# Kernel tuning notes

Measured on AMD Instinct MI355X. Metric: run time of the kernel, lower is better.

The kernel has to match this reference:

```python
import jax, jax.numpy as jnp
import numpy as np

D_MODEL = 1024
NUM_HEADS = 16
HEAD_DIM = D_MODEL // NUM_HEADS


def setup_inputs() -> dict:
    key = jax.random.key(0)
    ks = jax.random.split(key, 9)
    s = 1.0 / np.sqrt(D_MODEL)
    x = jax.random.normal(ks[0], (2, 2048, D_MODEL), dtype=jnp.float32)
    Wq = jax.random.uniform(ks[1], (D_MODEL, D_MODEL), jnp.float32, -s, s)
    bq = jax.random.uniform(ks[2], (D_MODEL,), jnp.float32, -s, s)
    Wk = jax.random.uniform(ks[3], (D_MODEL, D_MODEL), jnp.float32, -s, s)
    bk = jax.random.uniform(ks[4], (D_MODEL,), jnp.float32, -s, s)
    Wv = jax.random.uniform(ks[5], (D_MODEL, D_MODEL), jnp.float32, -s, s)
    bv = jax.random.uniform(ks[6], (D_MODEL,), jnp.float32, -s, s)
    Wo = jax.random.uniform(ks[7], (D_MODEL, D_MODEL), jnp.float32, -s, s)
    bo = jax.random.uniform(ks[8], (D_MODEL,), jnp.float32, -s, s)
    return {"x": x, "Wq": Wq, "bq": bq, "Wk": Wk, "bk": bk,
            "Wv": Wv, "bv": bv, "Wo": Wo, "bo": bo}


def reference(x, Wq, bq, Wk, bk, Wv, bv, Wo, bo):
    B, S, D = x.shape
    H, Hd = NUM_HEADS, HEAD_DIM
    # projections (torch Linear: x @ W.T + b; here W stored as [in, out])
    q = (x @ Wq + bq).reshape(B, S, H, Hd).transpose(0, 2, 1, 3)  # [B,H,S,Hd]
    k = (x @ Wk + bk).reshape(B, S, H, Hd).transpose(0, 2, 1, 3)
    v = (x @ Wv + bv).reshape(B, S, H, Hd).transpose(0, 2, 1, 3)
    scale = 1.0 / jnp.sqrt(jnp.asarray(Hd, dtype=x.dtype))
    scores = jnp.einsum('bhqd,bhkd->bhqk', q, k) * scale  # [B,H,S,S]
    attn = jax.nn.softmax(scores, axis=-1)
    out = jnp.einsum('bhqk,bhkd->bhqd', attn, v)  # [B,H,S,Hd]
    out = out.transpose(0, 2, 1, 3).reshape(B, S, D)
    return out @ Wo + bo
```

## Files before the change

kernel.cpp:

```cpp
#include <hip/hip_runtime.h>
#include <hip/hip_bf16.h>
#include <string.h>


#define DM 1024
#define S_LEN 2048
#define NH 16
#define HD 64

using u16 = unsigned short;
using u32 = unsigned int;

typedef short bf16x8 __attribute__((ext_vector_type(8)));
typedef float f32x4  __attribute__((ext_vector_type(4)));

__device__ __forceinline__ u16 f2bf(float f) {
    u32 i = __float_as_uint(f);
    u32 r = i + 0x7fffu + ((i >> 16) & 1u);
    return (u16)(r >> 16);
}
__device__ __forceinline__ u32 pk_bf16(float a, float b) {
    __hip_bfloat162 h = __float22bfloat162_rn(float2{a, b});
    u32 r; memcpy(&r, &h, 4);
    return r;
}

__global__ __launch_bounds__(256) void prep_x(const float* __restrict__ X, u16* __restrict__ out) {
    int i = (blockIdx.x * 256 + threadIdx.x) * 4;
    float4 v = *(const float4*)(X + i);
    *(uint2*)(out + i) = make_uint2(pk_bf16(v.x, v.y), pk_bf16(v.z, v.w));
}

__global__ __launch_bounds__(256) void prep_wt3(
    const float* __restrict__ W0, const float* __restrict__ W1, const float* __restrict__ W2,
    u16* __restrict__ T0, u16* __restrict__ T1, u16* __restrict__ T2)
{
    __shared__ u16 tile[64][72];
    const float* W = (blockIdx.z == 0) ? W0 : (blockIdx.z == 1) ? W1 : W2;
    u16* WT        = (blockIdx.z == 0) ? T0 : (blockIdx.z == 1) ? T1 : T2;
    const int t = threadIdx.x;
    const int n0 = blockIdx.x * 64, k0 = blockIdx.y * 64;
    #pragma unroll
    for (int it = 0; it < 4; it++) {
        int k = it * 16 + (t >> 4);
        int n = (t & 15) * 4;
        float4 v = *(const float4*)(W + (size_t)(k0 + k) * DM + n0 + n);
        tile[n + 0][k] = f2bf(v.x);
        tile[n + 1][k] = f2bf(v.y);
        tile[n + 2][k] = f2bf(v.z);
        tile[n + 3][k] = f2bf(v.w);
    }
    __syncthreads();
    int n = t >> 2, kg = (t & 3) * 16;
    uint4 a = *(const uint4*)&tile[n][kg];
    uint4 b = *(const uint4*)&tile[n][kg + 8];
    *(uint4*)(WT + (size_t)(n0 + n) * DM + k0 + kg)     = a;
    *(uint4*)(WT + (size_t)(n0 + n) * DM + k0 + kg + 8) = b;
}

__global__ __launch_bounds__(256) void prep_wt1(const float* __restrict__ W, u16* __restrict__ WT) {
    __shared__ u16 tile[64][72];
    const int t = threadIdx.x;
    const int n0 = blockIdx.x * 64, k0 = blockIdx.y * 64;
    #pragma unroll
    for (int it = 0; it < 4; it++) {
        int k = it * 16 + (t >> 4);
        int n = (t & 15) * 4;
        float4 v = *(const float4*)(W + (size_t)(k0 + k) * DM + n0 + n);
        tile[n + 0][k] = f2bf(v.x);
        tile[n + 1][k] = f2bf(v.y);
        tile[n + 2][k] = f2bf(v.z);
        tile[n + 3][k] = f2bf(v.w);
    }
    __syncthreads();
    int n = t >> 2, kg = (t & 3) * 16;
    uint4 a = *(const uint4*)&tile[n][kg];
    uint4 b = *(const uint4*)&tile[n][kg + 8];
    *(uint4*)(WT + (size_t)(n0 + n) * DM + k0 + kg)     = a;
    *(uint4*)(WT + (size_t)(n0 + n) * DM + k0 + kg + 8) = b;
}

__global__ __launch_bounds__(256) void gemm_qkv(
    const u16* __restrict__ WQT, const u16* __restrict__ WKT, const u16* __restrict__ WVT,
    const u16* __restrict__ X,
    const float* __restrict__ bq, const float* __restrict__ bk, const float* __restrict__ bv,
    u16* __restrict__ outQ, u16* __restrict__ outK, u16* __restrict__ outVT)
{
    __shared__ u16 Xs[128][72];
    __shared__ u16 Ws[3][64][72];

    const int t = threadIdx.x;
    const int w = t >> 6, lane = t & 63, quad = lane >> 4, l16 = lane & 15;
    const int Mb0 = blockIdx.x * 64;
    const int Nb0 = blockIdx.y * 128;
    const int Mb = Mb0 + (w & 1) * 32;
    const int Nb = Nb0 + (w >> 1) * 64;
    const int mloc = (w & 1) * 32, nloc = (w >> 1) * 64;

    f32x4 acc[3][2][4];
    #pragma unroll
    for (int q = 0; q < 3; q++)
        #pragma unroll
        for (int i = 0; i < 2; i++)
            #pragma unroll
            for (int j = 0; j < 4; j++) acc[q][i][j] = (f32x4){0.f, 0.f, 0.f, 0.f};

    const int sr = t >> 3, sc8 = (t & 7) * 8;

    for (int k0 = 0; k0 < DM; k0 += 64) {
        __syncthreads();
        #pragma unroll
        for (int i = 0; i < 4; i++) {
            int r = i * 32 + sr;
            *(uint4*)&Xs[r][sc8] =
                *(const uint4*)(X + (size_t)(Nb0 + r) * DM + k0 + sc8);
        }
        #pragma unroll
        for (int i = 0; i < 2; i++) {
            int r = i * 32 + sr;
            *(uint4*)&Ws[0][r][sc8] = *(const uint4*)(WQT + (size_t)(Mb0 + r) * DM + k0 + sc8);
            *(uint4*)&Ws[1][r][sc8] = *(const uint4*)(WKT + (size_t)(Mb0 + r) * DM + k0 + sc8);
            *(uint4*)&Ws[2][r][sc8] = *(const uint4*)(WVT + (size_t)(Mb0 + r) * DM + k0 + sc8);
        }
        __syncthreads();

        #pragma unroll
        for (int ks = 0; ks < 2; ks++) {
            const int kk = ks * 32 + quad * 8;
            bf16x8 bf[4];
            #pragma unroll
            for (int nt = 0; nt < 4; nt++)
                bf[nt] = *(const bf16x8*)&Xs[nloc + nt * 16 + l16][kk];
            bf16x8 aq0 = *(const bf16x8*)&Ws[0][mloc + l16][kk];
            bf16x8 aq1 = *(const bf16x8*)&Ws[0][mloc + 16 + l16][kk];
            bf16x8 ak0 = *(const bf16x8*)&Ws[1][mloc + l16][kk];
            bf16x8 ak1 = *(const bf16x8*)&Ws[1][mloc + 16 + l16][kk];
            bf16x8 av0 = *(const bf16x8*)&Ws[2][mloc + l16][kk];
            bf16x8 av1 = *(const bf16x8*)&Ws[2][mloc + 16 + l16][kk];
            #pragma unroll
            for (int nt = 0; nt < 4; nt++) {
                acc[0][0][nt] = __builtin_amdgcn_mfma_f32_16x16x32_bf16(aq0, bf[nt], acc[0][0][nt], 0, 0, 0);
                acc[0][1][nt] = __builtin_amdgcn_mfma_f32_16x16x32_bf16(aq1, bf[nt], acc[0][1][nt], 0, 0, 0);
                acc[1][0][nt] = __builtin_amdgcn_mfma_f32_16x16x32_bf16(ak0, bf[nt], acc[1][0][nt], 0, 0, 0);
                acc[1][1][nt] = __builtin_amdgcn_mfma_f32_16x16x32_bf16(ak1, bf[nt], acc[1][1][nt], 0, 0, 0);
                acc[2][0][nt] = __builtin_amdgcn_mfma_f32_16x16x32_bf16(av0, bf[nt], acc[2][0][nt], 0, 0, 0);
                acc[2][1][nt] = __builtin_amdgcn_mfma_f32_16x16x32_bf16(av1, bf[nt], acc[2][1][nt], 0, 0, 0);
            }
        }
    }

    const float QS = 0.18033688f;
    #pragma unroll
    for (int mt = 0; mt < 2; mt++) {
        int nf0 = Mb + mt * 16 + quad * 4;
        int h = nf0 >> 6, hd = nf0 & 63;
        float4 bvq = *(const float4*)(bq + nf0);
        float4 bvk = *(const float4*)(bk + nf0);
        #pragma unroll
        for (int nt = 0; nt < 4; nt++) {
            int m = Nb + nt * 16 + l16;
            int b = m >> 11, s = m & 2047;
            size_t idx = (size_t)(b * NH + h) * 131072 + (size_t)s * 64 + hd;
            *(uint2*)(outQ + idx) = make_uint2(
                pk_bf16((acc[0][mt][nt][0] + bvq.x) * QS, (acc[0][mt][nt][1] + bvq.y) * QS),
                pk_bf16((acc[0][mt][nt][2] + bvq.z) * QS, (acc[0][mt][nt][3] + bvq.w) * QS));
            *(uint2*)(outK + idx) = make_uint2(
                pk_bf16(acc[1][mt][nt][0] + bvk.x, acc[1][mt][nt][1] + bvk.y),
                pk_bf16(acc[1][mt][nt][2] + bvk.z, acc[1][mt][nt][3] + bvk.w));
        }
    }
    #pragma unroll
    for (int mt = 0; mt < 2; mt++) {
        #pragma unroll
        for (int r = 0; r < 4; r++) {
            int nf = Mb + mt * 16 + quad * 4 + r;
            int h = nf >> 6, hd = nf & 63;
            float bb = bv[nf];
            #pragma unroll
            for (int nt = 0; nt < 4; nt++) {
                int m = Nb + nt * 16 + l16;
                int b = m >> 11, s = m & 2047;
                outVT[(size_t)(b * NH + h) * 131072 + (size_t)hd * S_LEN + s]
                    = f2bf(acc[2][mt][nt][r] + bb);
            }
        }
    }
}

__global__ __launch_bounds__(256) void gemm_out(
    const u16* __restrict__ A, const u16* __restrict__ B,
    const float* __restrict__ bias, float* __restrict__ of32)
{
    __shared__ u16 As[64][72];
    __shared__ u16 Bs[128][72];

    const int t = threadIdx.x;
    const int w = t >> 6, lane = t & 63, quad = lane >> 4, l16 = lane & 15;
    const int Mb0 = blockIdx.x * 64;
    const int Nb0 = blockIdx.y * 128;
    const int Mb = Mb0 + (w & 1) * 32;
    const int Nb = Nb0 + (w >> 1) * 64;
    const int mloc = (w & 1) * 32, nloc = (w >> 1) * 64;

    f32x4 acc[2][4];
    #pragma unroll
    for (int i = 0; i < 2; i++)
        #pragma unroll
        for (int j = 0; j < 4; j++) acc[i][j] = (f32x4){0.f, 0.f, 0.f, 0.f};

    const int sr = t >> 3, sc8 = (t & 7) * 8;

    for (int k0 = 0; k0 < DM; k0 += 64) {
        const int h = k0 >> 6;
        __syncthreads();
        #pragma unroll
        for (int i = 0; i < 2; i++) {
            int r = i * 32 + sr;
            *(uint4*)&As[r][sc8] = *(const uint4*)(A + (size_t)(Mb0 + r) * DM + k0 + sc8);
        }
        #pragma unroll
        for (int i = 0; i < 4; i++) {
            int r = i * 32 + sr;
            int m = Nb0 + r;
            int b = m >> 11, s = m & 2047;
            *(uint4*)&Bs[r][sc8] =
                *(const uint4*)(B + (size_t)(b * NH + h) * 131072 + (size_t)s * 64 + sc8);
        }
        __syncthreads();

        #pragma unroll
        for (int ks = 0; ks < 2; ks++) {
            const int kk = ks * 32 + quad * 8;
            bf16x8 a0 = *(const bf16x8*)&As[mloc + l16][kk];
            bf16x8 a1 = *(const bf16x8*)&As[mloc + 16 + l16][kk];
            #pragma unroll
            for (int nt = 0; nt < 4; nt++) {
                bf16x8 bf = *(const bf16x8*)&Bs[nloc + nt * 16 + l16][kk];
                acc[0][nt] = __builtin_amdgcn_mfma_f32_16x16x32_bf16(a0, bf, acc[0][nt], 0, 0, 0);
                acc[1][nt] = __builtin_amdgcn_mfma_f32_16x16x32_bf16(a1, bf, acc[1][nt], 0, 0, 0);
            }
        }
    }
    #pragma unroll
    for (int mt = 0; mt < 2; mt++) {
        int nf0 = Mb + mt * 16 + quad * 4;
        float4 bvv = *(const float4*)(bias + nf0);
        #pragma unroll
        for (int nt = 0; nt < 4; nt++) {
            int m = Nb + nt * 16 + l16;
            float4 o;
            o.x = acc[mt][nt][0] + bvv.x; o.y = acc[mt][nt][1] + bvv.y;
            o.z = acc[mt][nt][2] + bvv.z; o.w = acc[mt][nt][3] + bvv.w;
            *(float4*)(of32 + (size_t)m * DM + nf0) = o;
        }
    }
}

__global__ __launch_bounds__(512) void attn_mfma(
    const u16* __restrict__ Q, const u16* __restrict__ K, const u16* __restrict__ VT,
    u16* __restrict__ O)
{
    __shared__ u16 Ks[2][64][72];
    __shared__ u16 Vs[2][64][72];
    __shared__ u16 P[128][72];

    const int t = threadIdx.x;
    const int w = t >> 6, lane = t & 63, quad = lane >> 4, l16 = lane & 15;
    const int bh = blockIdx.y;
    const int q0 = blockIdx.x * 128;
    const size_t base = (size_t)bh * 131072;

    bf16x8 qf[2];
    qf[0] = *(const bf16x8*)(Q + base + (size_t)(q0 + w * 16 + l16) * 64 + quad * 8);
    qf[1] = *(const bf16x8*)(Q + base + (size_t)(q0 + w * 16 + l16) * 64 + 32 + quad * 8);

    const short onebf = (short)0x3F80;
    const bf16x8 ones = {onebf, onebf, onebf, onebf, onebf, onebf, onebf, onebf};

    f32x4 o[4], lacc;
    #pragma unroll
    for (int i = 0; i < 4; i++) o[i] = (f32x4){0.f, 0.f, 0.f, 0.f};
    lacc = (f32x4){0.f, 0.f, 0.f, 0.f};

    const int sr = t >> 3;
    const int sc8 = (t & 7) * 8;
    const u16* Kg = K + base;
    const u16* Vg = VT + base;

    {
        uint4 k0v = *(const uint4*)(Kg + (size_t)sr * 64 + sc8);
        uint4 v0v = *(const uint4*)(Vg + (size_t)sr * S_LEN + sc8);
        *(uint4*)&Ks[0][sr][sc8] = k0v;
        *(uint4*)&Vs[0][sr][sc8] = v0v;
    }
    __syncthreads();

    uint4 kreg, vreg;
    for (int kt = 0; kt < 32; kt++) {
        const int cur = kt & 1;
        if (kt < 31) {
            kreg = *(const uint4*)(Kg + (size_t)((kt + 1) * 64 + sr) * 64 + sc8);
            vreg = *(const uint4*)(Vg + (size_t)sr * S_LEN + (kt + 1) * 64 + sc8);
        }

        f32x4 sc[4];
        #pragma unroll
        for (int i = 0; i < 4; i++) sc[i] = (f32x4){0.f, 0.f, 0.f, 0.f};
        #pragma unroll
        for (int ks = 0; ks < 2; ks++)
            #pragma unroll
            for (int nt = 0; nt < 4; nt++) {
                bf16x8 kf = *(const bf16x8*)&Ks[cur][nt * 16 + l16][ks * 32 + quad * 8];
                sc[nt] = __builtin_amdgcn_mfma_f32_16x16x32_bf16(qf[ks], kf, sc[nt], 0, 0, 0);
            }

        #pragma unroll
        for (int nt = 0; nt < 4; nt++) {
            float p0 = __builtin_amdgcn_exp2f(sc[nt][0]);
            float p1 = __builtin_amdgcn_exp2f(sc[nt][1]);
            float p2 = __builtin_amdgcn_exp2f(sc[nt][2]);
            float p3 = __builtin_amdgcn_exp2f(sc[nt][3]);
            u32 w01 = pk_bf16(p0, p1);
            u32 w23 = pk_bf16(p2, p3);
            const int row = w * 16 + quad * 4;
            const int col = nt * 16 + l16;
            P[row + 0][col] = (u16)(w01 & 0xffffu);
            P[row + 1][col] = (u16)(w01 >> 16);
            P[row + 2][col] = (u16)(w23 & 0xffffu);
            P[row + 3][col] = (u16)(w23 >> 16);
        }

        #pragma unroll
        for (int ks = 0; ks < 2; ks++) {
            bf16x8 pf = *(const bf16x8*)(&P[w * 16 + l16][ks * 32 + quad * 8]);
            lacc = __builtin_amdgcn_mfma_f32_16x16x32_bf16(pf, ones, lacc, 0, 0, 0);
            #pragma unroll
            for (int nt = 0; nt < 4; nt++) {
                bf16x8 vf = *(const bf16x8*)&Vs[cur][nt * 16 + l16][ks * 32 + quad * 8];
                o[nt] = __builtin_amdgcn_mfma_f32_16x16x32_bf16(pf, vf, o[nt], 0, 0, 0);
            }
        }

        if (kt < 31) {
            *(uint4*)&Ks[cur ^ 1][sr][sc8] = kreg;
            *(uint4*)&Vs[cur ^ 1][sr][sc8] = vreg;
        }
        __syncthreads();
    }

    #pragma unroll
    for (int r = 0; r < 4; r++) {
        float inv = 1.0f / lacc[r];
        int s = q0 + w * 16 + quad * 4 + r;
        #pragma unroll
        for (int nt = 0; nt < 4; nt++)
            O[base + (size_t)s * 64 + nt * 16 + l16] = f2bf(o[nt][r] * inv);
    }
}

extern "C" void kernel_launch(void* const* d_in, const int* in_sizes, int n_in,
                              void* d_out, int out_size, void* d_ws, size_t ws_size,
                              hipStream_t stream) {
    const float* x  = (const float*)d_in[0];
    const float* Wq = (const float*)d_in[1];
    const float* bq = (const float*)d_in[2];
    const float* Wk = (const float*)d_in[3];
    const float* bk = (const float*)d_in[4];
    const float* Wv = (const float*)d_in[5];
    const float* bv = (const float*)d_in[6];
    const float* Wo = (const float*)d_in[7];
    const float* bo = (const float*)d_in[8];
    float* out = (float*)d_out;

    u16* xbf = (u16*)d_out;
    u16* wqt = xbf + 4194304;
    u16* wkt = wqt + 1048576;
    u16* wvt = wkt + 1048576;

    u16* qws  = (u16*)d_ws;
    u16* kws  = qws + 4194304;
    u16* vtws = kws + 4194304;
    u16* wot  = kws;

    prep_x<<<4096, 256, 0, stream>>>(x, xbf);
    prep_wt3<<<dim3(16, 16, 3), 256, 0, stream>>>(Wq, Wk, Wv, wqt, wkt, wvt);

    gemm_qkv<<<dim3(16, 32), 256, 0, stream>>>(wqt, wkt, wvt, xbf, bq, bk, bv,
                                               qws, kws, vtws);

    attn_mfma<<<dim3(16, 32), 512, 0, stream>>>(qws, kws, vtws, qws);

    prep_wt1<<<dim3(16, 16), 256, 0, stream>>>(Wo, wot);
    gemm_out<<<dim3(16, 32), 256, 0, stream>>>(wot, qws, bo, out);
}
```

Baseline: 214.0 us.

## Switch attention to 32x32 MFMA with permlane swap instead of LDS P staging

```diff
diff --git a/kernel.cpp b/kernel.cpp
--- a/kernel.cpp
+++ b/kernel.cpp
@@ -13,6 +13,8 @@
 
 typedef short bf16x8 __attribute__((ext_vector_type(8)));
 typedef float f32x4  __attribute__((ext_vector_type(4)));
+typedef float f32x16 __attribute__((ext_vector_type(16)));
+typedef unsigned int u32x2 __attribute__((ext_vector_type(2)));
 
 __device__ __forceinline__ u16 f2bf(float f) {
     u32 i = __float_as_uint(f);
@@ -262,25 +264,30 @@
 {
     __shared__ u16 Ks[2][64][72];
     __shared__ u16 Vs[2][64][72];
-    __shared__ u16 P[128][72];
 
     const int t = threadIdx.x;
-    const int w = t >> 6, lane = t & 63, quad = lane >> 4, l16 = lane & 15;
+    const int w = t >> 6, lane = t & 63;
+    const int l32 = lane & 31, h = lane >> 5;
     const int bh = blockIdx.y;
-    const int q0 = blockIdx.x * 128;
+    const int q0 = blockIdx.x * 256;
     const size_t base = (size_t)bh * 131072;
 
-    bf16x8 qf[2];
-    qf[0] = *(const bf16x8*)(Q + base + (size_t)(q0 + w * 16 + l16) * 64 + quad * 8);
-    qf[1] = *(const bf16x8*)(Q + base + (size_t)(q0 + w * 16 + l16) * 64 + 32 + quad * 8);
+    const int qrow = q0 + w * 32 + l32;
+    bf16x8 qf[4];
+    #pragma unroll
+    for (int ks = 0; ks < 4; ks++)
+        qf[ks] = *(const bf16x8*)(Q + base + (size_t)qrow * 64 + ks * 16 + h * 8);
 
     const short onebf = (short)0x3F80;
     const bf16x8 ones = {onebf, onebf, onebf, onebf, onebf, onebf, onebf, onebf};
 
-    f32x4 o[4], lacc;
-    #pragma unroll
-    for (int i = 0; i < 4; i++) o[i] = (f32x4){0.f, 0.f, 0.f, 0.f};
-    lacc = (f32x4){0.f, 0.f, 0.f, 0.f};
+    f32x16 o[2], lacc;
+    #pragma unroll
+    for (int ht = 0; ht < 2; ht++)
+        #pragma unroll
+        for (int i = 0; i < 16; i++) o[ht][i] = 0.f;
+    #pragma unroll
+    for (int i = 0; i < 16; i++) lacc[i] = 0.f;
 
     const int sr = t >> 3;
     const int sc8 = (t & 7) * 8;
@@ -295,49 +302,48 @@
     }
     __syncthreads();
 
-    uint4 kreg, vreg;
     for (int kt = 0; kt < 32; kt++) {
         const int cur = kt & 1;
+        uint4 kreg, vreg;
         if (kt < 31) {
             kreg = *(const uint4*)(Kg + (size_t)((kt + 1) * 64 + sr) * 64 + sc8);
             vreg = *(const uint4*)(Vg + (size_t)sr * S_LEN + (kt + 1) * 64 + sc8);
         }
 
-        f32x4 sc[4];
-        #pragma unroll
-        for (int i = 0; i < 4; i++) sc[i] = (f32x4){0.f, 0.f, 0.f, 0.f};
-        #pragma unroll
-        for (int ks = 0; ks < 2; ks++)
-            #pragma unroll
-            for (int nt = 0; nt < 4; nt++) {
-                bf16x8 kf = *(const bf16x8*)&Ks[cur][nt * 16 + l16][ks * 32 + quad * 8];
-                sc[nt] = __builtin_amdgcn_mfma_f32_16x16x32_bf16(qf[ks], kf, sc[nt], 0, 0, 0);
+        #pragma unroll
+        for (int kh = 0; kh < 2; kh++) {
+            f32x16 s;
+            #pragma unroll
+            for (int i = 0; i < 16; i++) s[i] = 0.f;
+            #pragma unroll
+            for (int ks = 0; ks < 4; ks++) {
+                bf16x8 kf = *(const bf16x8*)&Ks[cur][kh * 32 + l32][ks * 16 + h * 8];
+                s = __builtin_amdgcn_mfma_f32_32x32x16_bf16(kf, qf[ks], s, 0, 0, 0);
             }
-
-        #pragma unroll
-        for (int nt = 0; nt < 4; nt++) {
-            float p0 = __builtin_amdgcn_exp2f(sc[nt][0]);
-            float p1 = __builtin_amdgcn_exp2f(sc[nt][1]);
-            float p2 = __builtin_amdgcn_exp2f(sc[nt][2]);
-            float p3 = __builtin_amdgcn_exp2f(sc[nt][3]);
-            u32 w01 = pk_bf16(p0, p1);
-            u32 w23 = pk_bf16(p2, p3);
-            const int row = w * 16 + quad * 4;
-            const int col = nt * 16 + l16;
-            P[row + 0][col] = (u16)(w01 & 0xffffu);
-            P[row + 1][col] = (u16)(w01 >> 16);
-            P[row + 2][col] = (u16)(w23 & 0xffffu);
-            P[row + 3][col] = (u16)(w23 >> 16);
-        }
-
-        #pragma unroll
-        for (int ks = 0; ks < 2; ks++) {
-            bf16x8 pf = *(const bf16x8*)(&P[w * 16 + l16][ks * 32 + quad * 8]);
-            lacc = __builtin_amdgcn_mfma_f32_16x16x32_bf16(pf, ones, lacc, 0, 0, 0);
-            #pragma unroll
-            for (int nt = 0; nt < 4; nt++) {
-                bf16x8 vf = *(const bf16x8*)&Vs[cur][nt * 16 + l16][ks * 32 + quad * 8];
-                o[nt] = __builtin_amdgcn_mfma_f32_16x16x32_bf16(pf, vf, o[nt], 0, 0, 0);
+            float p[16];
+            #pragma unroll
+            for (int i = 0; i < 16; i++) p[i] = __builtin_amdgcn_exp2f(s[i]);
+            u32 A0 = pk_bf16(p[0],  p[1]),  B0 = pk_bf16(p[2],  p[3]);
+            u32 A1 = pk_bf16(p[4],  p[5]),  B1 = pk_bf16(p[6],  p[7]);
+            u32 A2 = pk_bf16(p[8],  p[9]),  B2 = pk_bf16(p[10], p[11]);
+            u32 A3 = pk_bf16(p[12], p[13]), B3 = pk_bf16(p[14], p[15]);
+            u32x2 sA0 = __builtin_amdgcn_permlane32_swap(A0, A1, false, false);
+            u32x2 sB0 = __builtin_amdgcn_permlane32_swap(B0, B1, false, false);
+            u32x2 sA1 = __builtin_amdgcn_permlane32_swap(A2, A3, false, false);
+            u32x2 sB1 = __builtin_amdgcn_permlane32_swap(B2, B3, false, false);
+            union { bf16x8 v; u32 wd[4]; } fr0, fr1;
+            fr0.wd[0] = sA0.x; fr0.wd[1] = sB0.x; fr0.wd[2] = sA0.y; fr0.wd[3] = sB0.y;
+            fr1.wd[0] = sA1.x; fr1.wd[1] = sB1.x; fr1.wd[2] = sA1.y; fr1.wd[3] = sB1.y;
+
+            lacc = __builtin_amdgcn_mfma_f32_32x32x16_bf16(fr0.v, ones, lacc, 0, 0, 0);
+            lacc = __builtin_amdgcn_mfma_f32_32x32x16_bf16(fr1.v, ones, lacc, 0, 0, 0);
+
+            #pragma unroll
+            for (int ht = 0; ht < 2; ht++) {
+                bf16x8 vf0 = *(const bf16x8*)&Vs[cur][ht * 32 + l32][kh * 32 + h * 8];
+                o[ht] = __builtin_amdgcn_mfma_f32_32x32x16_bf16(fr0.v, vf0, o[ht], 0, 0, 0);
+                bf16x8 vf1 = *(const bf16x8*)&Vs[cur][ht * 32 + l32][kh * 32 + 16 + h * 8];
+                o[ht] = __builtin_amdgcn_mfma_f32_32x32x16_bf16(fr1.v, vf1, o[ht], 0, 0, 0);
             }
         }
 
@@ -348,14 +354,16 @@
         __syncthreads();
     }
 
-    #pragma unroll
-    for (int r = 0; r < 4; r++) {
-        float inv = 1.0f / lacc[r];
-        int s = q0 + w * 16 + quad * 4 + r;
-        #pragma unroll
-        for (int nt = 0; nt < 4; nt++)
-            O[base + (size_t)s * 64 + nt * 16 + l16] = f2bf(o[nt][r] * inv);
-    }
+    float inv[16];
+    #pragma unroll
+    for (int r = 0; r < 16; r++) inv[r] = 1.0f / lacc[r];
+    #pragma unroll
+    for (int ht = 0; ht < 2; ht++)
+        #pragma unroll
+        for (int r = 0; r < 16; r++) {
+            int q = q0 + w * 32 + (r & 3) + 8 * (r >> 2) + 4 * h;
+            O[base + (size_t)q * 64 + ht * 32 + l32] = f2bf(o[ht][r] * inv[r]);
+        }
 }
 
 extern "C" void kernel_launch(void* const* d_in, const int* in_sizes, int n_in,
@@ -388,7 +396,7 @@
     gemm_qkv<<<dim3(16, 32), 256, 0, stream>>>(wqt, wkt, wvt, xbf, bq, bk, bv,
                                                qws, kws, vtws);
 
-    attn_mfma<<<dim3(16, 32), 512, 0, stream>>>(qws, kws, vtws, qws);
+    attn_mfma<<<dim3(8, 32), 512, 0, stream>>>(qws, kws, vtws, qws);
 
     prep_wt1<<<dim3(16, 16), 256, 0, stream>>>(Wo, wot);
     gemm_out<<<dim3(16, 32), 256, 0, stream>>>(wot, qws, bo, out);
```

New measurement: 200.9 us. 6.1% less time.
